# Performance work log

Measured on AMD Instinct MI355X. Metric: run time of the kernel, lower is better.

## Reference

```python
import jax, jax.numpy as jnp
import numpy as np

D_MODEL = 1024
NUM_HEADS = 16
HEAD_DIM = D_MODEL // NUM_HEADS
THETA = 10000.0
B, T = 2, 2048


def setup_inputs() -> dict:
    key = jax.random.key(0)
    k1, k2, k3 = jax.random.split(key, 3)
    x = jax.random.normal(k1, (B, T, D_MODEL), dtype=jnp.float32)
    W_qkv = jax.random.normal(k2, (3 * D_MODEL, D_MODEL), dtype=jnp.float32) * 0.02
    W_o = jax.random.normal(k3, (D_MODEL, D_MODEL), dtype=jnp.float32) * 0.02
    return {"x": x, "W_qkv": W_qkv, "W_o": W_o}


def _rope(x, cos, sin):
    # x: [B, h, T, d]; rotate interleaved even/odd pairs
    x_even = x[..., 0::2]
    x_odd = x[..., 1::2]
    out_even = x_even * cos - x_odd * sin
    out_odd = x_even * sin + x_odd * cos
    out = jnp.stack([out_even, out_odd], axis=-1)  # [B,h,T,d/2,2]
    return out.reshape(x.shape)


def reference(x, W_qkv, W_o):
    b, t, dm = x.shape
    # fused QKV projection (bias-free Linear: x @ W.T)
    qkv = jnp.einsum('btd,ed->bte', x, W_qkv)                # [B,T,3*D]
    qkv = qkv.reshape(b, t, 3, NUM_HEADS, HEAD_DIM)
    qkv = jnp.transpose(qkv, (2, 0, 3, 1, 4))                # [3,B,h,T,d]
    q, k, v = qkv[0], qkv[1], qkv[2]

    # RoPE with token_positions = arange(T)
    pos = jnp.arange(t, dtype=jnp.float32)                   # [T]
    inv_freq = THETA ** (-jnp.arange(0, HEAD_DIM, 2, dtype=jnp.float32) / HEAD_DIM)
    ang = pos[:, None] * inv_freq[None, :]                   # [T, d/2]
    cos = jnp.cos(ang)[None, None, :, :]
    sin = jnp.sin(ang)[None, None, :, :]
    q = _rope(q, cos, sin)
    k = _rope(k, cos, sin)

    # causal scaled dot-product attention
    scale = 1.0 / jnp.sqrt(jnp.asarray(HEAD_DIM, dtype=x.dtype))
    scores = jnp.einsum('bhqd,bhkd->bhqk', q, k) * scale     # [B,h,T,T]
    causal = jnp.tril(jnp.ones((t, t), dtype=bool))
    scores = jnp.where(causal[None, None, :, :], scores, -jnp.inf)
    attn = jax.nn.softmax(scores, axis=-1)
    out = jnp.einsum('bhqk,bhkd->bhqd', attn, v)             # [B,h,T,d]
    out = jnp.transpose(out, (0, 2, 1, 3)).reshape(b, t, dm) # [B,T,D]
    return jnp.einsum('btd,ed->bte', out, W_o)
```

## Files before the change

### kernel.cpp

```cpp
#include <hip/hip_runtime.h>
#include <hip/hip_bf16.h>
#include <cstdint>

#define NHEADS 16
#define HDIM 64
#define BB 2
#define TSEQ 2048
#define DM 1024
#define MROWS (BB*TSEQ)

typedef unsigned short u16;
typedef unsigned int u32;
typedef __bf16 bf16x8 __attribute__((ext_vector_type(8)));
typedef float f32x4 __attribute__((ext_vector_type(4)));

#define AS1C(p) ((const __attribute__((address_space(1))) u32*)(p))
#define AS3(p)  ((__attribute__((address_space(3))) u32*)(p))

static __device__ __forceinline__ u16 f2bf(float f) {
  return __builtin_bit_cast(u16, __float2bfloat16(f));
}
static __device__ __forceinline__ float bf2f(u16 u) {
  return __bfloat162float(__builtin_bit_cast(__hip_bfloat16, u));
}
static __device__ __forceinline__ u32 pack2bf(float a, float b) {
  const u32 ua = __builtin_bit_cast(u32, a) + 0x8000u;
  const u32 ub = __builtin_bit_cast(u32, b) + 0x8000u;
  return (ua >> 16) | (ub & 0xFFFF0000u);
}
static __device__ __forceinline__ f32x4 mfma16x16(bf16x8 a, bf16x8 b, f32x4 c) {
  return __builtin_amdgcn_mfma_f32_16x16x32_bf16(a, b, c, 0, 0, 0);
}

#define N4_X   (MROWS * DM / 4)
#define N4_WQ  (3 * DM * DM / 4)
#define N4_WO  (DM * DM / 4)
__global__ __launch_bounds__(256) void cast_all(const float* __restrict__ x,
                                                const float* __restrict__ wq,
                                                const float* __restrict__ wo,
                                                u16* __restrict__ xb,
                                                u16* __restrict__ wqb,
                                                u16* __restrict__ wob) {
  int i = blockIdx.x * 256 + threadIdx.x;
  const int stride = gridDim.x * 256;
  for (; i < N4_X + N4_WQ + N4_WO; i += stride) {
    const float4* src; u16* dst; int j;
    if (i < N4_X)            { src = (const float4*)x;  dst = xb;  j = i; }
    else if (i < N4_X + N4_WQ) { src = (const float4*)wq; dst = wqb; j = i - N4_X; }
    else                     { src = (const float4*)wo; dst = wob; j = i - N4_X - N4_WQ; }
    float4 v = src[j];
    ushort4 o;
    o.x = f2bf(v.x); o.y = f2bf(v.y); o.z = f2bf(v.z); o.w = f2bf(v.w);
    ((ushort4*)dst)[j] = o;
  }
}

template<int WRITE_BF16>
__global__ __launch_bounds__(256, 2) void gemm_bt(const u16* __restrict__ A,
                                                  const u16* __restrict__ Bm,
                                                  float* __restrict__ Cf,
                                                  u16* __restrict__ Cb,
                                                  int M, int N, int K) {
  __shared__ u16 lA[2][128 * 32];
  __shared__ u16 lB[2][128 * 32];
  const int tid = threadIdx.x;
  const int w = tid >> 6, l = tid & 63;
  const int wr = w >> 1, wc = w & 1;
  int bid = blockIdx.y * gridDim.x + blockIdx.x;
  const int cpx = (gridDim.x * gridDim.y) >> 3;
  bid = (bid & 7) * cpx + (bid >> 3);
  const int bx = bid % gridDim.x, by = bid / gridDim.x;
  const int brow = by * 128, bcol = bx * 128;
  const int lr = l & 15, lg = l >> 4;

  const int srow = l >> 2;
  const int scol = (((l & 3) ^ (srow & 3)) * 8);

  auto stage = [&](int buf, int k0) {
#pragma unroll
    for (int is = 0; is < 2; ++is) {
      const int chunk = w * 2 + is;
      const int row = chunk * 16 + srow;
      __builtin_amdgcn_global_load_lds(AS1C(A + (size_t)(brow + row) * K + k0 + scol),
                                       AS3((char*)lA[buf] + chunk * 1024), 16, 0, 0);
      __builtin_amdgcn_global_load_lds(AS1C(Bm + (size_t)(bcol + row) * K + k0 + scol),
                                       AS3((char*)lB[buf] + chunk * 1024), 16, 0, 0);
    }
  };

  f32x4 acc[4][4] = {};
  const int nk = K >> 5;
  stage(0, 0);
  for (int kk = 0; kk < nk; ++kk) {
    const int cur = kk & 1;
    __syncthreads();
    if (kk + 1 < nk) stage(cur ^ 1, (kk + 1) << 5);
    bf16x8 af[4], bfr[4];
#pragma unroll
    for (int m = 0; m < 4; ++m) {
      const int row = wr * 64 + m * 16 + lr;
      const int sl = lg ^ (row & 3);
      af[m] = *(const bf16x8*)(&lA[cur][row * 32 + sl * 8]);
    }
#pragma unroll
    for (int n = 0; n < 4; ++n) {
      const int row = wc * 64 + n * 16 + lr;
      const int sl = lg ^ (row & 3);
      bfr[n] = *(const bf16x8*)(&lB[cur][row * 32 + sl * 8]);
    }
#pragma unroll
    for (int m = 0; m < 4; ++m)
#pragma unroll
      for (int n = 0; n < 4; ++n)
        acc[m][n] = mfma16x16(af[m], bfr[n], acc[m][n]);
  }
#pragma unroll
  for (int m = 0; m < 4; ++m)
#pragma unroll
    for (int n = 0; n < 4; ++n)
#pragma unroll
      for (int r = 0; r < 4; ++r) {
        const int row = brow + wr * 64 + m * 16 + lg * 4 + r;
        const int col = bcol + wc * 64 + n * 16 + lr;
        if constexpr (WRITE_BF16)
          Cb[(size_t)row * N + col] = f2bf(acc[m][n][r]);
        else
          Cf[(size_t)row * N + col] = acc[m][n][r];
      }
}

__global__ __launch_bounds__(256) void rope_reshape(const u16* __restrict__ qkvb,
                                                    u16* __restrict__ qb,
                                                    u16* __restrict__ kb,
                                                    u16* __restrict__ vbT) {
  const int bh = blockIdx.y;
  const int b = bh >> 4, h = bh & 15;
  const int t0 = blockIdx.x * 64;
  const int tid = threadIdx.x;
  const float C = -0.4152410118609203f;
  const float QS = 0.125f * 1.44269504088896341f;

  for (int idx = tid; idx < 64 * 32; idx += 256) {
    const int tl = idx >> 5, p = idx & 31;
    const int t = t0 + tl;
    const size_t base = ((size_t)(b * TSEQ + t)) * 3072 + h * 64 + 2 * p;
    const float qe = bf2f(qkvb[base]), qo = bf2f(qkvb[base + 1]);
    const float ke = bf2f(qkvb[base + 1024]), ko = bf2f(qkvb[base + 1025]);
    const float inv = exp2f((float)p * C);
    const float ang = (float)t * inv;
    float sn, cs;
    sincosf(ang, &sn, &cs);
    const size_t ob = ((size_t)bh * TSEQ + t) * 64 + 2 * p;
    qb[ob]     = f2bf((qe * cs - qo * sn) * QS);
    qb[ob + 1] = f2bf((qe * sn + qo * cs) * QS);
    kb[ob]     = f2bf(ke * cs - ko * sn);
    kb[ob + 1] = f2bf(ke * sn + ko * cs);
  }

  __shared__ u16 lT[64][65];
  for (int idx = tid; idx < 64 * 64; idx += 256) {
    const int tl = idx >> 6, d = idx & 63;
    lT[tl][d] = qkvb[((size_t)(b * TSEQ + t0 + tl)) * 3072 + 2048 + h * 64 + d];
  }
  __syncthreads();
  for (int idx = tid; idx < 64 * 64; idx += 256) {
    const int d = idx >> 6, tl = idx & 63;
    vbT[((size_t)bh * 64 + d) * TSEQ + t0 + tl] = lT[tl][d];
  }
}

__global__ __launch_bounds__(256, 2) void attn_fwd(const u16* __restrict__ qb,
                                                   const u16* __restrict__ kb,
                                                   const u16* __restrict__ vbT,
                                                   u16* __restrict__ ob) {
  __shared__ u16 lK[2][2][64 * 64];
  __shared__ u16 lV[2][2][64 * 64];
  __shared__ u16 lP[4][16 * 64];
  const int hw = blockIdx.x;
  const int logical = (hw & 7) * 64 + (hw >> 3);
  const int bh = logical >> 4;
  const int pair = logical & 15;
  const int b = bh >> 4, h = bh & 15;
  const int tid = threadIdx.x;
  const int w = tid >> 6, l = tid & 63;
  const int g = w >> 1, wq = w & 1;
  const int lr = l & 15, lg = l >> 4;
  const int srow8 = l >> 3;
  const int scol = ((l & 7) ^ srow8) * 8;
  const u16* Kb = kb + (size_t)bh * TSEQ * 64;
  const u16* Vb = vbT + (size_t)bh * 64 * TSEQ;
  u16* lPw = lP[w];

  auto stage = [&](int buf, int kt) {
#pragma unroll
    for (int is = 0; is < 4; ++is) {
      const int chunk = wq * 4 + is;
      const int row = chunk * 8 + srow8;
      __builtin_amdgcn_global_load_lds(AS1C(Kb + (size_t)(kt * 64 + row) * 64 + scol),
                                       AS3((char*)lK[g][buf] + chunk * 1024), 16, 0, 0);
      __builtin_amdgcn_global_load_lds(AS1C(Vb + (size_t)row * TSEQ + kt * 64 + scol),
                                       AS3((char*)lV[g][buf] + chunk * 1024), 16, 0, 0);
    }
  };

  for (int half = 0; half < 2; ++half) {
    const int qt = half ? (31 - pair) : pair;
    const int q0 = qt * 64;
    const int nt = qt + 1;
    const int nit = (nt + 1) >> 1;
    const int qa0 = q0 + wq * 32 + lr;

    bf16x8 qf[2][2];
    {
      const u16* qp = qb + ((size_t)bh * TSEQ + q0 + wq * 32 + lr) * 64 + lg * 8;
      qf[0][0] = *(const bf16x8*)qp;
      qf[0][1] = *(const bf16x8*)(qp + 32);
      qp += 16 * 64;
      qf[1][0] = *(const bf16x8*)qp;
      qf[1][1] = *(const bf16x8*)(qp + 32);
    }

    f32x4 o0[4] = {}, o1[4] = {};
    float ls0 = 0.f, ls1 = 0.f;

    __syncthreads();
    if (g < nt) stage(0, g);
    for (int it = 0; it < nit; ++it) {
      const int cur = it & 1;
      __syncthreads();
      const int ktn = 2 * (it + 1) + g;
      if (ktn < nt) stage(cur ^ 1, ktn);
      const int kt = 2 * it + g;
      if (kt < nt) {
        const u16* Kc = lK[g][cur];
        const u16* Vc = lV[g][cur];

        f32x4 s0[4] = {}, s1[4] = {};
        __builtin_amdgcn_s_setprio(1);
#pragma unroll
        for (int n = 0; n < 4; ++n) {
          const int row = n * 16 + lr;
#pragma unroll
          for (int ks = 0; ks < 2; ++ks) {
            const int sl = (ks * 4 + lg) ^ (row & 7);
            bf16x8 kf = *(const bf16x8*)(&Kc[row * 64 + sl * 8]);
            s0[n] = mfma16x16(kf, qf[0][ks], s0[n]);
            s1[n] = mfma16x16(kf, qf[1][ks], s1[n]);
          }
        }
        __builtin_amdgcn_s_setprio(0);

        const bool diag = (kt == qt);
        const int kvb = kt * 64;

#pragma unroll
        for (int n = 0; n < 4; ++n) {
          float pv[4];
#pragma unroll
          for (int r = 0; r < 4; ++r) {
            float p = __builtin_amdgcn_exp2f(s0[n][r]);
            if (diag && (kvb + n * 16 + lg * 4 + r > qa0)) p = 0.f;
            pv[r] = p;
            ls0 += p;
          }
          const int phys = (n * 2 + (lg >> 1)) ^ (lr & 7);
          uint2 pk; pk.x = pack2bf(pv[0], pv[1]); pk.y = pack2bf(pv[2], pv[3]);
          *(uint2*)(&lPw[lr * 64 + phys * 8 + (lg & 1) * 4]) = pk;
        }
        bf16x8 pf0[2];
#pragma unroll
        for (int ks = 0; ks < 2; ++ks) {
          const int phys = (ks * 4 + lg) ^ (lr & 7);
          pf0[ks] = *(const bf16x8*)(&lPw[lr * 64 + phys * 8]);
        }

#pragma unroll
        for (int n = 0; n < 4; ++n) {
          float pv[4];
#pragma unroll
          for (int r = 0; r < 4; ++r) {
            float p = __builtin_amdgcn_exp2f(s1[n][r]);
            if (diag && (kvb + n * 16 + lg * 4 + r > qa0 + 16)) p = 0.f;
            pv[r] = p;
            ls1 += p;
          }
          const int phys = (n * 2 + (lg >> 1)) ^ (lr & 7);
          uint2 pk; pk.x = pack2bf(pv[0], pv[1]); pk.y = pack2bf(pv[2], pv[3]);
          *(uint2*)(&lPw[lr * 64 + phys * 8 + (lg & 1) * 4]) = pk;
        }
        bf16x8 pf1[2];
#pragma unroll
        for (int ks = 0; ks < 2; ++ks) {
          const int phys = (ks * 4 + lg) ^ (lr & 7);
          pf1[ks] = *(const bf16x8*)(&lPw[lr * 64 + phys * 8]);
        }

        __builtin_amdgcn_s_setprio(1);
#pragma unroll
        for (int n = 0; n < 4; ++n) {
          const int row = n * 16 + lr;
#pragma unroll
          for (int ks = 0; ks < 2; ++ks) {
            const int sl = (ks * 4 + lg) ^ (row & 7);
            bf16x8 vf = *(const bf16x8*)(&Vc[row * 64 + sl * 8]);
            o0[n] = mfma16x16(vf, pf0[ks], o0[n]);
            o1[n] = mfma16x16(vf, pf1[ks], o1[n]);
          }
        }
        __builtin_amdgcn_s_setprio(0);
      }
    }

    ls0 += __shfl_xor(ls0, 16); ls0 += __shfl_xor(ls0, 32);
    ls1 += __shfl_xor(ls1, 16); ls1 += __shfl_xor(ls1, 32);

    __syncthreads();
    float* mO = (float*)&lK[0][0][0];
    float* mL = (float*)&lV[0][0][0];
    if (g == 1) {
#pragma unroll
      for (int qs = 0; qs < 2; ++qs)
#pragma unroll
        for (int n = 0; n < 4; ++n)
#pragma unroll
          for (int r = 0; r < 4; ++r) {
            const int d = n * 16 + lg * 4 + r;
            mO[((wq * 2 + qs) * 64 + d) * 16 + lr] = (qs ? o1[n][r] : o0[n][r]);
          }
      if (lg == 0) {
        mL[(wq * 2 + 0) * 16 + lr] = ls0;
        mL[(wq * 2 + 1) * 16 + lr] = ls1;
      }
    }
    __syncthreads();
    if (g == 0) {
      const float rl0 = 1.f / (ls0 + mL[(wq * 2 + 0) * 16 + lr]);
      const float rl1 = 1.f / (ls1 + mL[(wq * 2 + 1) * 16 + lr]);
#pragma unroll
      for (int qs = 0; qs < 2; ++qs) {
        const int q = q0 + wq * 32 + qs * 16 + lr;
        const float rl = qs ? rl1 : rl0;
#pragma unroll
        for (int n = 0; n < 4; ++n) {
          ushort4 ov;
#pragma unroll
          for (int r = 0; r < 4; ++r) {
            const int d = n * 16 + lg * 4 + r;
            const float o = (qs ? o1[n][r] : o0[n][r]) + mO[((wq * 2 + qs) * 64 + d) * 16 + lr];
            ((u16*)&ov)[r] = f2bf(o * rl);
          }
          *(ushort4*)(&ob[(size_t)(b * TSEQ + q) * DM + h * 64 + n * 16 + lg * 4]) = ov;
        }
      }
    }
  }
}

extern "C" void kernel_launch(void* const* d_in, const int* in_sizes, int n_in,
                              void* d_out, int out_size, void* d_ws, size_t ws_size,
                              hipStream_t stream) {
  const float* x    = (const float*)d_in[0];
  const float* Wqkv = (const float*)d_in[1];
  const float* Wo   = (const float*)d_in[2];
  float* out = (float*)d_out;

  char* ws = (char*)d_ws;
  u16* xb    = (u16*)ws; ws += (size_t)MROWS * DM * 2;
  u16* wqkvb = (u16*)ws; ws += (size_t)3 * DM * DM * 2;
  u16* wob   = (u16*)ws; ws += (size_t)DM * DM * 2;
  u16* qkvb  = (u16*)ws; ws += (size_t)MROWS * 3 * DM * 2;
  u16* qb    = (u16*)ws; ws += (size_t)BB * NHEADS * TSEQ * HDIM * 2;
  u16* kb    = (u16*)ws; ws += (size_t)BB * NHEADS * TSEQ * HDIM * 2;
  u16* vbT   = (u16*)ws; ws += (size_t)BB * NHEADS * TSEQ * HDIM * 2;
  u16* ob    = (u16*)ws; ws += (size_t)MROWS * DM * 2;

  cast_all<<<2048, 256, 0, stream>>>(x, Wqkv, Wo, xb, wqkvb, wob);

  gemm_bt<1><<<dim3(3 * DM / 128, MROWS / 128), 256, 0, stream>>>(
      xb, wqkvb, nullptr, qkvb, MROWS, 3 * DM, DM);

  rope_reshape<<<dim3(TSEQ / 64, BB * NHEADS), 256, 0, stream>>>(qkvb, qb, kb, vbT);

  attn_fwd<<<512, 256, 0, stream>>>(qb, kb, vbT, ob);

  gemm_bt<0><<<dim3(DM / 128, MROWS / 128), 256, 0, stream>>>(
      ob, wob, out, nullptr, MROWS, DM, DM);
}
```

Measured before the change: 115.6 us.

## Halve attention KV tile to 32 and raise occupancy to four blocks per CU

The attention kernel now processes 32-key tiles instead of 64, shrinking the K/V/P LDS buffers and rewriting staging, swizzles, and MFMA loops for that size. The causal diagonal is handled per 32-row query subgroup, so each warp skips key tiles that are fully masked for its rows. Launch bounds move from 2 to 4 blocks per CU to improve latency hiding. In exchange, each tile carries less work relative to its barrier and loop overhead, there are more iterations, and registers are capped tighter, which risks spills.

```diff
diff --git a/kernel.cpp b/kernel.cpp
--- a/kernel.cpp
+++ b/kernel.cpp
@@ -169,13 +169,13 @@
   }
 }
 
-__global__ __launch_bounds__(256, 2) void attn_fwd(const u16* __restrict__ qb,
+__global__ __launch_bounds__(256, 4) void attn_fwd(const u16* __restrict__ qb,
                                                    const u16* __restrict__ kb,
                                                    const u16* __restrict__ vbT,
                                                    u16* __restrict__ ob) {
-  __shared__ u16 lK[2][2][64 * 64];
-  __shared__ u16 lV[2][2][64 * 64];
-  __shared__ u16 lP[4][16 * 64];
+  __shared__ u16 lK[2][2][32 * 64];
+  __shared__ u16 lV[2][2][64 * 32];
+  __shared__ u16 lP[4][16 * 40];
   const int hw = blockIdx.x;
   const int logical = (hw & 7) * 64 + (hw >> 3);
   const int bh = logical >> 4;
@@ -185,20 +185,21 @@
   const int w = tid >> 6, l = tid & 63;
   const int g = w >> 1, wq = w & 1;
   const int lr = l & 15, lg = l >> 4;
-  const int srow8 = l >> 3;
-  const int scol = ((l & 7) ^ srow8) * 8;
+  const int kscol = ((l & 7) ^ (l >> 3)) * 8;
+  const int vscol = ((l & 3) ^ ((l >> 2) & 3)) * 8;
   const u16* Kb = kb + (size_t)bh * TSEQ * 64;
   const u16* Vb = vbT + (size_t)bh * 64 * TSEQ;
   u16* lPw = lP[w];
 
   auto stage = [&](int buf, int kt) {
 #pragma unroll
-    for (int is = 0; is < 4; ++is) {
-      const int chunk = wq * 4 + is;
-      const int row = chunk * 8 + srow8;
-      __builtin_amdgcn_global_load_lds(AS1C(Kb + (size_t)(kt * 64 + row) * 64 + scol),
+    for (int is = 0; is < 2; ++is) {
+      const int chunk = wq * 2 + is;
+      const int krow = chunk * 8 + (l >> 3);
+      __builtin_amdgcn_global_load_lds(AS1C(Kb + (size_t)(kt * 32 + krow) * 64 + kscol),
                                        AS3((char*)lK[g][buf] + chunk * 1024), 16, 0, 0);
-      __builtin_amdgcn_global_load_lds(AS1C(Vb + (size_t)row * TSEQ + kt * 64 + scol),
+      const int vrow = chunk * 16 + (l >> 2);
+      __builtin_amdgcn_global_load_lds(AS1C(Vb + (size_t)vrow * TSEQ + kt * 32 + vscol),
                                        AS3((char*)lV[g][buf] + chunk * 1024), 16, 0, 0);
     }
   };
@@ -206,8 +207,7 @@
   for (int half = 0; half < 2; ++half) {
     const int qt = half ? (31 - pair) : pair;
     const int q0 = qt * 64;
-    const int nt = qt + 1;
-    const int nit = (nt + 1) >> 1;
+    const int ts = 2 * qt + wq;
     const int qa0 = q0 + wq * 32 + lr;
 
     bf16x8 qf[2][2];
@@ -224,37 +224,40 @@
     float ls0 = 0.f, ls1 = 0.f;
 
     __syncthreads();
-    if (g < nt) stage(0, g);
-    for (int it = 0; it < nit; ++it) {
+    stage(0, g);
+    for (int it = 0; it <= qt; ++it) {
       const int cur = it & 1;
       __syncthreads();
-      const int ktn = 2 * (it + 1) + g;
-      if (ktn < nt) stage(cur ^ 1, ktn);
+      if (it < qt) stage(cur ^ 1, 2 * (it + 1) + g);
       const int kt = 2 * it + g;
-      if (kt < nt) {
+      if (kt <= ts) {
         const u16* Kc = lK[g][cur];
         const u16* Vc = lV[g][cur];
 
-        f32x4 s0[4] = {}, s1[4] = {};
+        bf16x8 kf[2][2];
+#pragma unroll
+        for (int n = 0; n < 2; ++n) {
+          const int row = n * 16 + lr;
+#pragma unroll
+          for (int ks = 0; ks < 2; ++ks)
+            kf[n][ks] = *(const bf16x8*)(&Kc[row * 64 + (((ks * 4 + lg) ^ (row & 7)) * 8)]);
+        }
+        f32x4 s0[2] = {}, s1[2] = {};
         __builtin_amdgcn_s_setprio(1);
 #pragma unroll
-        for (int n = 0; n < 4; ++n) {
-          const int row = n * 16 + lr;
+        for (int n = 0; n < 2; ++n)
 #pragma unroll
           for (int ks = 0; ks < 2; ++ks) {
-            const int sl = (ks * 4 + lg) ^ (row & 7);
-            bf16x8 kf = *(const bf16x8*)(&Kc[row * 64 + sl * 8]);
-            s0[n] = mfma16x16(kf, qf[0][ks], s0[n]);
-            s1[n] = mfma16x16(kf, qf[1][ks], s1[n]);
-          }
-        }
+            s0[n] = mfma16x16(kf[n][ks], qf[0][ks], s0[n]);
+            s1[n] = mfma16x16(kf[n][ks], qf[1][ks], s1[n]);
+          }
         __builtin_amdgcn_s_setprio(0);
 
-        const bool diag = (kt == qt);
-        const int kvb = kt * 64;
-
-#pragma unroll
-        for (int n = 0; n < 4; ++n) {
+        const bool diag = (kt == ts);
+        const int kvb = kt * 32;
+
+#pragma unroll
+        for (int n = 0; n < 2; ++n) {
           float pv[4];
 #pragma unroll
           for (int r = 0; r < 4; ++r) {
@@ -263,19 +266,13 @@
             pv[r] = p;
             ls0 += p;
           }
-          const int phys = (n * 2 + (lg >> 1)) ^ (lr & 7);
           uint2 pk; pk.x = pack2bf(pv[0], pv[1]); pk.y = pack2bf(pv[2], pv[3]);
-          *(uint2*)(&lPw[lr * 64 + phys * 8 + (lg & 1) * 4]) = pk;
-        }
-        bf16x8 pf0[2];
-#pragma unroll
-        for (int ks = 0; ks < 2; ++ks) {
-          const int phys = (ks * 4 + lg) ^ (lr & 7);
-          pf0[ks] = *(const bf16x8*)(&lPw[lr * 64 + phys * 8]);
-        }
-
-#pragma unroll
-        for (int n = 0; n < 4; ++n) {
+          *(uint2*)(&lPw[lr * 40 + n * 16 + lg * 4]) = pk;
+        }
+        bf16x8 pf0 = *(const bf16x8*)(&lPw[lr * 40 + lg * 8]);
+
+#pragma unroll
+        for (int n = 0; n < 2; ++n) {
           float pv[4];
 #pragma unroll
           for (int r = 0; r < 4; ++r) {
@@ -284,28 +281,18 @@
             pv[r] = p;
             ls1 += p;
           }
-          const int phys = (n * 2 + (lg >> 1)) ^ (lr & 7);
           uint2 pk; pk.x = pack2bf(pv[0], pv[1]); pk.y = pack2bf(pv[2], pv[3]);
-          *(uint2*)(&lPw[lr * 64 + phys * 8 + (lg & 1) * 4]) = pk;
-        }
-        bf16x8 pf1[2];
-#pragma unroll
-        for (int ks = 0; ks < 2; ++ks) {
-          const int phys = (ks * 4 + lg) ^ (lr & 7);
-          pf1[ks] = *(const bf16x8*)(&lPw[lr * 64 + phys * 8]);
-        }
+          *(uint2*)(&lPw[lr * 40 + n * 16 + lg * 4]) = pk;
+        }
+        bf16x8 pf1 = *(const bf16x8*)(&lPw[lr * 40 + lg * 8]);
 
         __builtin_amdgcn_s_setprio(1);
 #pragma unroll
         for (int n = 0; n < 4; ++n) {
           const int row = n * 16 + lr;
-#pragma unroll
-          for (int ks = 0; ks < 2; ++ks) {
-            const int sl = (ks * 4 + lg) ^ (row & 7);
-            bf16x8 vf = *(const bf16x8*)(&Vc[row * 64 + sl * 8]);
-            o0[n] = mfma16x16(vf, pf0[ks], o0[n]);
-            o1[n] = mfma16x16(vf, pf1[ks], o1[n]);
-          }
+          bf16x8 vf = *(const bf16x8*)(&Vc[row * 32 + ((lg ^ (row & 3)) * 8)]);
+          o0[n] = mfma16x16(vf, pf0, o0[n]);
+          o1[n] = mfma16x16(vf, pf1, o1[n]);
         }
         __builtin_amdgcn_s_setprio(0);
       }
```

Measured after the change: 121.3 us. +4.9%, slower.
